# Optimization experiments

Measured on AMD Instinct MI355X. Metric: run time of the kernel, lower is better.

Reference implementation:

```python
import jax, jax.numpy as jnp
import numpy as np

K_MASK = -2.3819763e+38
B, T, D = 1, 2048, 3584
N, KH, H = 28, 4, 128  # query heads, kv heads, head_dim
ROPE_THETA = 1000000.0


def _rope_tables(t, h, theta):
    pos = jnp.arange(t, dtype=jnp.float32)[:, None]
    freq = theta ** (-jnp.arange(0, h, 2, dtype=jnp.float32) / h)[None, :]
    ang = pos * freq  # (T, H/2)
    return jnp.sin(ang)[None], jnp.cos(ang)[None]  # (1, T, H/2)


def apply_rotary_embedding(x, sin, cos):
    # x: (B,T,heads,H); sin/cos: (B,T,H/2)
    x1, x2 = x[..., : x.shape[-1] // 2], x[..., x.shape[-1] // 2 :]
    s, c = sin[:, :, None, :], cos[:, :, None, :]
    return jnp.concatenate([x1 * c - x2 * s, x2 * c + x1 * s], axis=-1)


def setup_inputs() -> dict:
    key = jax.random.key(0)
    ks = jax.random.split(key, 8)
    x = jax.random.normal(ks[0], (B, T, D), jnp.float32)
    attn_mask = jnp.tril(jnp.ones((T, T), jnp.bool_))[None]  # causal (B,T,S)
    sin, cos = _rope_tables(T, H, ROPE_THETA)
    std = 0.02
    wq = jax.random.normal(ks[1], (D, N, H), jnp.float32) * std
    wk = jax.random.normal(ks[2], (D, KH, H), jnp.float32) * std
    wv = jax.random.normal(ks[3], (D, KH, H), jnp.float32) * std
    wo = jax.random.normal(ks[4], (N, H, D), jnp.float32) * std
    q_bias = jax.random.normal(ks[5], (N * H,), jnp.float32) * std
    k_bias = jax.random.normal(ks[6], (KH * H,), jnp.float32) * std
    v_bias = jax.random.normal(ks[7], (KH * H,), jnp.float32) * std
    return {"x": x, "attn_mask": attn_mask, "sin": sin, "cos": cos,
            "wq": wq, "wk": wk, "wv": wv, "wo": wo,
            "q_bias": q_bias, "k_bias": k_bias, "v_bias": v_bias}


def reference(x, attn_mask, sin, cos, wq, wk, wv, wo, q_bias, k_bias, v_bias):
    b, t, _ = x.shape
    q = jnp.einsum('BTD,DNH->BTNH', x, wq) + q_bias.reshape(1, 1, N, H)
    k = jnp.einsum('BSD,DKH->BSKH', x, wk) + k_bias.reshape(1, 1, KH, H)
    v = jnp.einsum('BSD,DKH->BSKH', x, wv) + v_bias.reshape(1, 1, KH, H)
    q = apply_rotary_embedding(q, sin, cos)
    k = apply_rotary_embedding(k, sin, cos)
    g = N // KH  # GQA group size
    scale = H ** -0.5
    qg = q.reshape(b, t, KH, g, H)
    attn = jnp.einsum('BTHGD,BSHD->BHGTS', qg, k) * scale  # no KV repetition
    attn = attn.reshape(b, N, t, t)
    attn = jnp.where(attn_mask[:, None, :, :], attn, K_MASK)
    attn = jax.nn.softmax(attn.astype(jnp.float32), axis=-1).astype(k.dtype)
    attn = attn.reshape(b, KH, g, t, t)
    qkv = jnp.einsum('BHGTS,BSHD->BTHGD', attn, v).reshape(b, t, N, H)
    return jnp.einsum('BTNH,NHD->BTD', qkv, wo)
```

## Files before the change

kernel.cpp:

```cpp
#include <hip/hip_runtime.h>
#include <hip/hip_bf16.h>
#include <math.h>

#define Tn 2048
#define Dn 3584
#define NH 28
#define KHn 4
#define Hn 128
#define Gn 7
#define SCALE 0.08838834764831845f
#define LDC 4608
#define KOFF 3584
#define VOFF 4096
#define FBQ 128
#define FBS 64
#define NSPLIT 2

typedef unsigned short u16;
typedef __attribute__((ext_vector_type(8))) short short8;
typedef __attribute__((ext_vector_type(4))) float floatx4;

__device__ __forceinline__ float bf_lo(unsigned int u) {
    union { unsigned int i; float f; } x; x.i = u << 16; return x.f;
}
__device__ __forceinline__ u16 f2bf(float f) {
    __hip_bfloat16 h = __float2bfloat16(f);
    return *reinterpret_cast<u16*>(&h);
}

__global__ void cast_f32_bf16(const float* __restrict__ in, u16* __restrict__ out, int n4)
{
    const int idx = blockIdx.x * blockDim.x + threadIdx.x;
    if (idx >= n4) return;
    const float4 f = ((const float4*)in)[idx];
    ((ushort4*)out)[idx] = make_ushort4(f2bf(f.x), f2bf(f.y), f2bf(f.z), f2bf(f.w));
}

__global__ __launch_bounds__(256) void transpose_cast(
    const float* __restrict__ in, u16* __restrict__ out, int R, int C, int ldo)
{
    __shared__ float ts[32][33];
    const int tid = threadIdx.x;
    const int c0 = blockIdx.x * 32, r0 = blockIdx.y * 32;
    const int tx = tid & 31, ty = tid >> 5;
    #pragma unroll
    for (int i = 0; i < 4; ++i)
        ts[ty + i * 8][tx] = in[(size_t)(r0 + ty + i * 8) * C + c0 + tx];
    __syncthreads();
    #pragma unroll
    for (int i = 0; i < 4; ++i)
        out[(size_t)(c0 + ty + i * 8) * ldo + r0 + tx] = f2bf(ts[tx][ty + i * 8]);
}

__global__ __launch_bounds__(256) void transpose_v(
    const u16* __restrict__ qkv, u16* __restrict__ vt)
{
    __shared__ u16 ts[32][33];
    const int tid = threadIdx.x;
    const int s0 = blockIdx.x * 32, d0 = blockIdx.y * 32;
    const int tx = tid & 31, ty = tid >> 5;
    #pragma unroll
    for (int i = 0; i < 4; ++i)
        ts[ty + i * 8][tx] = qkv[(size_t)(s0 + ty + i * 8) * LDC + VOFF + d0 + tx];
    __syncthreads();
    #pragma unroll
    for (int i = 0; i < 4; ++i)
        vt[(size_t)(d0 + ty + i * 8) * Tn + s0 + tx] = ts[tx][ty + i * 8];
}

__global__ void concat_bias(const float* __restrict__ qb, const float* __restrict__ kb,
                            const float* __restrict__ vb, float* __restrict__ out)
{
    const int j = blockIdx.x * blockDim.x + threadIdx.x;
    if (j >= 4608) return;
    out[j] = j < 3584 ? qb[j] : (j < 4096 ? kb[j - 3584] : vb[j - 4096]);
}

#define GM 128
#define GN 128
#define GK 32

__device__ __forceinline__ void async16(const void* g, void* l) {
    __builtin_amdgcn_global_load_lds(
        (const __attribute__((address_space(1))) unsigned int*)g,
        (__attribute__((address_space(3))) unsigned int*)l, 16, 0, 0);
}

template <typename OUT_T>
__global__ __launch_bounds__(256) void gemm_bf16_mfma(
    const u16* __restrict__ A, const u16* __restrict__ Bt,
    const float* __restrict__ bias, OUT_T* __restrict__ C,
    int M, int N, int K, int ldc)
{
    __shared__ __align__(16) u16 As[GM * GK];
    __shared__ __align__(16) u16 Bs[GN * GK];

    const int tid  = threadIdx.x;
    const int lane = tid & 63;
    const int wave = tid >> 6;
    const int wr = wave >> 1, wc = wave & 1;
    const int m16 = lane & 15, quad = lane >> 4;

    const int bm = blockIdx.y * GM;
    const int bn = blockIdx.x * GN;

    floatx4 acc[4][4];
    #pragma unroll
    for (int i = 0; i < 4; ++i)
        #pragma unroll
        for (int j = 0; j < 4; ++j) acc[i][j] = (floatx4)0.f;

    const int rl   = lane >> 2;
    const int kcol = (lane & 3) * 8;

    for (int k0 = 0; k0 < K; k0 += GK) {
        __syncthreads();
        #pragma unroll
        for (int i = 0; i < 2; ++i) {
            const int c = wave + i * 4;
            const int row = c * 16 + rl;
            async16(A  + (size_t)(bm + row) * K + k0 + kcol, &As[c * 512]);
            async16(Bt + (size_t)(bn + row) * K + k0 + kcol, &Bs[c * 512]);
        }
        __builtin_amdgcn_s_waitcnt(0);
        __syncthreads();

        short8 af[4], bfr[4];
        #pragma unroll
        for (int i = 0; i < 4; ++i)
            af[i] = *(const short8*)&As[(wr * 64 + i * 16 + m16) * GK + quad * 8];
        #pragma unroll
        for (int j = 0; j < 4; ++j)
            bfr[j] = *(const short8*)&Bs[(wc * 64 + j * 16 + m16) * GK + quad * 8];
        #pragma unroll
        for (int i = 0; i < 4; ++i)
            #pragma unroll
            for (int j = 0; j < 4; ++j)
                acc[i][j] = __builtin_amdgcn_mfma_f32_16x16x32_bf16(
                    af[i], bfr[j], acc[i][j], 0, 0, 0);
    }

    #pragma unroll
    for (int j = 0; j < 4; ++j) {
        const int col = bn + wc * 64 + j * 16 + m16;
        const float bv = bias ? bias[col] : 0.f;
        #pragma unroll
        for (int i = 0; i < 4; ++i) {
            const int rbase = bm + wr * 64 + i * 16 + quad * 4;
            #pragma unroll
            for (int r = 0; r < 4; ++r) {
                const float v = acc[i][j][r] + bv;
                if constexpr (sizeof(OUT_T) == 2)
                    C[(size_t)(rbase + r) * ldc + col] = (OUT_T)f2bf(v);
                else
                    C[(size_t)(rbase + r) * ldc + col] = v;
            }
        }
    }
}

__global__ void rope_bf16(u16* __restrict__ base,
                          const float* __restrict__ sin_t,
                          const float* __restrict__ cos_t,
                          int heads)
{
    const int idx = blockIdx.x * blockDim.x + threadIdx.x;
    const int n_elem = Tn * heads * 64;
    if (idx >= n_elem) return;
    const int i = idx & 63;
    const int h = (idx >> 6) % heads;
    const int t = idx / (64 * heads);
    const float s = sin_t[t * 64 + i];
    const float c = cos_t[t * 64 + i];
    u16* p = base + (size_t)t * LDC + h * Hn;
    const float x1 = bf_lo((unsigned int)p[i]);
    const float x2 = bf_lo((unsigned int)p[i + 64]);
    p[i]      = f2bf(x1 * c - x2 * s);
    p[i + 64] = f2bf(x2 * c + x1 * s);
}

__global__ __launch_bounds__(256, 2) void flash_attn_mfma(
    const u16* __restrict__ qkv, const u16* __restrict__ vt,
    float* __restrict__ po0, float* __restrict__ po1,
    float2* __restrict__ ml)
{
    const int qt = (int)(gridDim.x - 1 - blockIdx.x);
    const int n  = blockIdx.y;
    const int z  = blockIdx.z;
    const int kh = n / Gn;
    const int tid  = threadIdx.x;
    const int lane = tid & 63;
    const int w    = tid >> 6;
    const int m16  = lane & 15;
    const int quad = lane >> 4;

    __shared__ __align__(16) u16 smem[64 * 136 + 128 * 72 + 128 * 72];
    u16* Ks = smem;
    u16* Vs = smem + 64 * 136;
    u16* Ps = Vs + 128 * 72;

    short8 qf[2][4];
    #pragma unroll
    for (int p = 0; p < 2; ++p) {
        const int qrow = qt * FBQ + w * 32 + p * 16 + m16;
        const u16* qp = qkv + (size_t)qrow * LDC + n * Hn;
        #pragma unroll
        for (int kc = 0; kc < 4; ++kc)
            qf[p][kc] = *(const short8*)(qp + kc * 32 + quad * 8);
    }

    floatx4 oacc[2][8];
    #pragma unroll
    for (int p = 0; p < 2; ++p)
        #pragma unroll
        for (int jn = 0; jn < 8; ++jn) oacc[p][jn] = (floatx4)0.f;
    float mrow[2][4], lrow[2][4];
    #pragma unroll
    for (int p = 0; p < 2; ++p)
        #pragma unroll
        for (int r = 0; r < 4; ++r) { mrow[p][r] = -3.0e38f; lrow[p][r] = 0.f; }

    const int krow = tid >> 2, kseg = tid & 3;
    const int vrow = tid >> 1, vseg = tid & 1;
    const int st0 = z * (qt + 1);
    const int st1 = st0 + qt + 1;

    uint4 kv[4], vv[4];
    {
        const u16* kp = qkv + (size_t)(st0 * FBS + krow) * LDC + KOFF + kh * Hn + kseg * 32;
        #pragma unroll
        for (int i = 0; i < 4; ++i) kv[i] = *(const uint4*)(kp + i * 8);
        const u16* vp = vt + (size_t)(kh * Hn + vrow) * Tn + st0 * FBS + vseg * 32;
        #pragma unroll
        for (int i = 0; i < 4; ++i) vv[i] = *(const uint4*)(vp + i * 8);
    }

    for (int st = st0; st < st1; ++st) {
        __syncthreads();
        #pragma unroll
        for (int i = 0; i < 4; ++i)
            *(uint4*)&Ks[krow * 136 + kseg * 32 + i * 8] = kv[i];
        #pragma unroll
        for (int i = 0; i < 4; ++i)
            *(uint4*)&Vs[vrow * 72 + vseg * 32 + i * 8] = vv[i];
        __syncthreads();

        {
            const int pst = (st + 1 < st1) ? st + 1 : st1 - 1;
            const u16* kp = qkv + (size_t)(pst * FBS + krow) * LDC + KOFF + kh * Hn + kseg * 32;
            #pragma unroll
            for (int i = 0; i < 4; ++i) kv[i] = *(const uint4*)(kp + i * 8);
            const u16* vp = vt + (size_t)(kh * Hn + vrow) * Tn + pst * FBS + vseg * 32;
            #pragma unroll
            for (int i = 0; i < 4; ++i) vv[i] = *(const uint4*)(vp + i * 8);
        }

        const bool active = (st * FBS) <= (qt * FBQ + w * 32 + 31);
        if (active) {
            floatx4 sacc[2][4];
            #pragma unroll
            for (int p = 0; p < 2; ++p)
                #pragma unroll
                for (int j = 0; j < 4; ++j) sacc[p][j] = (floatx4)0.f;
            #pragma unroll
            for (int j = 0; j < 4; ++j) {
                #pragma unroll
                for (int kc = 0; kc < 4; ++kc) {
                    const short8 bfv = *(const short8*)&Ks[(j * 16 + m16) * 136 + kc * 32 + quad * 8];
                    sacc[0][j] = __builtin_amdgcn_mfma_f32_16x16x32_bf16(qf[0][kc], bfv, sacc[0][j], 0, 0, 0);
                    sacc[1][j] = __builtin_amdgcn_mfma_f32_16x16x32_bf16(qf[1][kc], bfv, sacc[1][j], 0, 0, 0);
                }
            }

            const bool diag = (st >= 2 * qt);
            #pragma unroll
            for (int p = 0; p < 2; ++p) {
                #pragma unroll
                for (int r = 0; r < 4; ++r) {
                    const int prow = w * 32 + p * 16 + quad * 4 + r;
                    const int row  = qt * FBQ + prow;
                    float sv[4];
                    #pragma unroll
                    for (int j = 0; j < 4; ++j) {
                        float s = sacc[p][j][r] * SCALE;
                        if (diag && (st * FBS + j * 16 + m16 > row)) s = -1.0e30f;
                        sv[j] = s;
                    }
                    float mx = fmaxf(fmaxf(sv[0], sv[1]), fmaxf(sv[2], sv[3]));
                    mx = fmaxf(mx, __shfl_xor(mx, 1));
                    mx = fmaxf(mx, __shfl_xor(mx, 2));
                    mx = fmaxf(mx, __shfl_xor(mx, 4));
                    mx = fmaxf(mx, __shfl_xor(mx, 8));
                    const float mnew  = fmaxf(mrow[p][r], mx);
                    const float alpha = __expf(mrow[p][r] - mnew);
                    mrow[p][r] = mnew;
                    float ls = 0.f;
                    #pragma unroll
                    for (int j = 0; j < 4; ++j) {
                        const float e = __expf(sv[j] - mnew);
                        ls += e;
                        Ps[prow * 72 + j * 16 + m16] = f2bf(e);
                    }
                    lrow[p][r] = lrow[p][r] * alpha + ls;
                    #pragma unroll
                    for (int jn = 0; jn < 8; ++jn) oacc[p][jn][r] *= alpha;
                }
            }

            #pragma unroll
            for (int kc2 = 0; kc2 < 2; ++kc2) {
                const short8 af0 = *(const short8*)&Ps[(w * 32 + m16) * 72 + kc2 * 32 + quad * 8];
                const short8 af1 = *(const short8*)&Ps[(w * 32 + 16 + m16) * 72 + kc2 * 32 + quad * 8];
                #pragma unroll
                for (int jn = 0; jn < 8; ++jn) {
                    const short8 bfv = *(const short8*)&Vs[(jn * 16 + m16) * 72 + kc2 * 32 + quad * 8];
                    oacc[0][jn] = __builtin_amdgcn_mfma_f32_16x16x32_bf16(af0, bfv, oacc[0][jn], 0, 0, 0);
                    oacc[1][jn] = __builtin_amdgcn_mfma_f32_16x16x32_bf16(af1, bfv, oacc[1][jn], 0, 0, 0);
                }
            }
        }
    }

    float lsum[2][4];
    #pragma unroll
    for (int p = 0; p < 2; ++p)
        #pragma unroll
        for (int r = 0; r < 4; ++r) {
            float l = lrow[p][r];
            l += __shfl_xor(l, 1); l += __shfl_xor(l, 2);
            l += __shfl_xor(l, 4); l += __shfl_xor(l, 8);
            lsum[p][r] = l;
        }

    if (m16 == 0) {
        #pragma unroll
        for (int p = 0; p < 2; ++p)
            #pragma unroll
            for (int r = 0; r < 4; ++r) {
                const int row = qt * FBQ + w * 32 + p * 16 + quad * 4 + r;
                ml[((size_t)z * NH + n) * Tn + row] = make_float2(mrow[p][r], lsum[p][r]);
            }
    }

    float* po = z ? po1 : po0;
    #pragma unroll
    for (int p = 0; p < 2; ++p)
        #pragma unroll
        for (int r = 0; r < 4; ++r) {
            const int grow = qt * FBQ + w * 32 + p * 16 + quad * 4 + r;
            float* pr = po + (size_t)grow * Dn + n * Hn + m16;
            #pragma unroll
            for (int jn = 0; jn < 8; ++jn)
                pr[jn * 16] = oacc[p][jn][r];
        }
}

__global__ __launch_bounds__(256) void combine_splits(
    const float* __restrict__ po0, const float* __restrict__ po1,
    const float2* __restrict__ ml, u16* __restrict__ ob)
{
    const int idx = blockIdx.x * blockDim.x + threadIdx.x;
    const int n4  = Tn * Dn / 4;
    if (idx >= n4) return;
    const int c4  = idx % (Dn / 4);
    const int row = idx / (Dn / 4);
    const int n   = (c4 * 4) / Hn;

    const float2 ml0 = ml[(size_t)n * Tn + row];
    const float2 ml1 = ml[(size_t)(NH + n) * Tn + row];
    const float  M   = fmaxf(ml0.x, ml1.x);
    const float  a0  = __expf(ml0.x - M);
    const float  a1  = __expf(ml1.x - M);
    const float  dn_ = 1.0f / (ml0.y * a0 + ml1.y * a1);

    const float4 v0 = ((const float4*)po0)[idx];
    const float4 v1 = ((const float4*)po1)[idx];
    ushort4 o;
    o.x = f2bf((v0.x * a0 + v1.x * a1) * dn_);
    o.y = f2bf((v0.y * a0 + v1.y * a1) * dn_);
    o.z = f2bf((v0.z * a0 + v1.z * a1) * dn_);
    o.w = f2bf((v0.w * a0 + v1.w * a1) * dn_);
    ((ushort4*)ob)[idx] = o;
}

extern "C" void kernel_launch(void* const* d_in, const int* in_sizes, int n_in,
                              void* d_out, int out_size, void* d_ws, size_t ws_size,
                              hipStream_t stream)
{
    const float* x      = (const float*)d_in[0];
    const float* sin_t  = (const float*)d_in[2];
    const float* cos_t  = (const float*)d_in[3];
    const float* wq     = (const float*)d_in[4];
    const float* wk     = (const float*)d_in[5];
    const float* wv     = (const float*)d_in[6];
    const float* wo     = (const float*)d_in[7];
    const float* q_bias = (const float*)d_in[8];
    const float* k_bias = (const float*)d_in[9];
    const float* v_bias = (const float*)d_in[10];
    float* out = (float*)d_out;

    char* ws = (char*)d_ws;
    u16*  cqkv = (u16*)ws;
    u16*  abuf = (u16*)(ws + 18874368);
    u16*  wt   = (u16*)(ws + 18874368 + 14680064);
    float* bqkv = (float*)(ws + 66584576);
    u16*  vtg  = wt;
    float* po0 = (float*)d_out;
    float* po1 = (float*)(ws + 35651584);
    float2* mlb = (float2*)(ws + 65011712);
    u16*  xb   = (u16*)d_out;

    cast_f32_bf16<<<(Tn * Dn / 4 + 255) / 256, 256, 0, stream>>>(x, xb, Tn * Dn / 4);
    transpose_cast<<<dim3(Dn / 32, Dn / 32), 256, 0, stream>>>(wq, wt, Dn, Dn, Dn);
    transpose_cast<<<dim3(512 / 32, Dn / 32), 256, 0, stream>>>(wk, wt + (size_t)KOFF * Dn, Dn, 512, Dn);
    transpose_cast<<<dim3(512 / 32, Dn / 32), 256, 0, stream>>>(wv, wt + (size_t)VOFF * Dn, Dn, 512, Dn);
    concat_bias<<<18, 256, 0, stream>>>(q_bias, k_bias, v_bias, bqkv);

    gemm_bf16_mfma<u16><<<dim3(LDC / GN, Tn / GM), 256, 0, stream>>>(
        xb, wt, bqkv, cqkv, Tn, LDC, Dn, LDC);

    rope_bf16<<<(Tn * 32 * 64 + 255) / 256, 256, 0, stream>>>(cqkv, sin_t, cos_t, 32);

    transpose_v<<<dim3(Tn / 32, 512 / 32), 256, 0, stream>>>(cqkv, vtg);

    flash_attn_mfma<<<dim3(Tn / FBQ, NH, NSPLIT), 256, 0, stream>>>(
        cqkv, vtg, po0, po1, mlb);

    combine_splits<<<(Tn * Dn / 4 + 255) / 256, 256, 0, stream>>>(po0, po1, mlb, abuf);

    transpose_cast<<<dim3(Dn / 32, Dn / 32), 256, 0, stream>>>(wo, wt, Dn, Dn, Dn);
    gemm_bf16_mfma<float><<<dim3(Dn / GN, Tn / GM), 256, 0, stream>>>(
        abuf, wt, nullptr, out, Tn, Dn, Dn, Dn);
}
```

Measured before the change: 621.0 us.

## Load K/V MFMA fragments directly from global memory, drop LDS staging

The flash attention kernel no longer stages K and V tiles through shared memory with register prefetch and two barriers per tile. Each wave now reads its MFMA B-operand fragments straight from global memory (relying on L1/L2 caching), keeping only the P tile in LDS. This removes the block-wide syncs and cuts LDS use, which could raise occupancy and let waves skip inactive tiles independently. The cost is that every wave refetches the same K/V data, the loads are strided and uncoalesced, and the software prefetch that hid their latency is gone.

```diff
diff --git a/kernel.cpp b/kernel.cpp
--- a/kernel.cpp
+++ b/kernel.cpp
@@ -194,10 +194,7 @@
     const int m16  = lane & 15;
     const int quad = lane >> 4;
 
-    __shared__ __align__(16) u16 smem[64 * 136 + 128 * 72 + 128 * 72];
-    u16* Ks = smem;
-    u16* Vs = smem + 64 * 136;
-    u16* Ps = Vs + 128 * 72;
+    __shared__ __align__(16) u16 Ps[128 * 72];
 
     short8 qf[2][4];
     #pragma unroll
@@ -220,103 +217,77 @@
         #pragma unroll
         for (int r = 0; r < 4; ++r) { mrow[p][r] = -3.0e38f; lrow[p][r] = 0.f; }
 
-    const int krow = tid >> 2, kseg = tid & 3;
-    const int vrow = tid >> 1, vseg = tid & 1;
     const int st0 = z * (qt + 1);
     const int st1 = st0 + qt + 1;
 
-    uint4 kv[4], vv[4];
-    {
-        const u16* kp = qkv + (size_t)(st0 * FBS + krow) * LDC + KOFF + kh * Hn + kseg * 32;
-        #pragma unroll
-        for (int i = 0; i < 4; ++i) kv[i] = *(const uint4*)(kp + i * 8);
-        const u16* vp = vt + (size_t)(kh * Hn + vrow) * Tn + st0 * FBS + vseg * 32;
-        #pragma unroll
-        for (int i = 0; i < 4; ++i) vv[i] = *(const uint4*)(vp + i * 8);
-    }
+    const u16* kfrag = qkv + (size_t)m16 * LDC + KOFF + kh * Hn + quad * 8;
+    const u16* vfrag = vt + (size_t)(kh * Hn + m16) * Tn + quad * 8;
 
     for (int st = st0; st < st1; ++st) {
-        __syncthreads();
-        #pragma unroll
-        for (int i = 0; i < 4; ++i)
-            *(uint4*)&Ks[krow * 136 + kseg * 32 + i * 8] = kv[i];
-        #pragma unroll
-        for (int i = 0; i < 4; ++i)
-            *(uint4*)&Vs[vrow * 72 + vseg * 32 + i * 8] = vv[i];
-        __syncthreads();
-
-        {
-            const int pst = (st + 1 < st1) ? st + 1 : st1 - 1;
-            const u16* kp = qkv + (size_t)(pst * FBS + krow) * LDC + KOFF + kh * Hn + kseg * 32;
-            #pragma unroll
-            for (int i = 0; i < 4; ++i) kv[i] = *(const uint4*)(kp + i * 8);
-            const u16* vp = vt + (size_t)(kh * Hn + vrow) * Tn + pst * FBS + vseg * 32;
-            #pragma unroll
-            for (int i = 0; i < 4; ++i) vv[i] = *(const uint4*)(vp + i * 8);
-        }
-
-        const bool active = (st * FBS) <= (qt * FBQ + w * 32 + 31);
-        if (active) {
-            floatx4 sacc[2][4];
-            #pragma unroll
-            for (int p = 0; p < 2; ++p)
+        if ((st * FBS) > (qt * FBQ + w * 32 + 31)) continue;
+
+        const u16* kb = kfrag + (size_t)(st * FBS) * LDC;
+        const u16* vb = vfrag + st * FBS;
+
+        floatx4 sacc[2][4];
+        #pragma unroll
+        for (int j = 0; j < 4; ++j) sacc[0][j] = (floatx4)0.f;
+        #pragma unroll
+        for (int j = 0; j < 4; ++j) sacc[1][j] = (floatx4)0.f;
+        #pragma unroll
+        for (int j = 0; j < 4; ++j) {
+            #pragma unroll
+            for (int kc = 0; kc < 4; ++kc) {
+                const short8 bfv = *(const short8*)(kb + (size_t)(j * 16) * LDC + kc * 32);
+                sacc[0][j] = __builtin_amdgcn_mfma_f32_16x16x32_bf16(qf[0][kc], bfv, sacc[0][j], 0, 0, 0);
+                sacc[1][j] = __builtin_amdgcn_mfma_f32_16x16x32_bf16(qf[1][kc], bfv, sacc[1][j], 0, 0, 0);
+            }
+        }
+
+        const bool diag = (st >= 2 * qt);
+        #pragma unroll
+        for (int p = 0; p < 2; ++p) {
+            #pragma unroll
+            for (int r = 0; r < 4; ++r) {
+                const int prow = w * 32 + p * 16 + quad * 4 + r;
+                const int row  = qt * FBQ + prow;
+                float sv[4];
                 #pragma unroll
-                for (int j = 0; j < 4; ++j) sacc[p][j] = (floatx4)0.f;
-            #pragma unroll
-            for (int j = 0; j < 4; ++j) {
+                for (int j = 0; j < 4; ++j) {
+                    float s = sacc[p][j][r] * SCALE;
+                    if (diag && (st * FBS + j * 16 + m16 > row)) s = -1.0e30f;
+                    sv[j] = s;
+                }
+                float mx = fmaxf(fmaxf(sv[0], sv[1]), fmaxf(sv[2], sv[3]));
+                mx = fmaxf(mx, __shfl_xor(mx, 1));
+                mx = fmaxf(mx, __shfl_xor(mx, 2));
+                mx = fmaxf(mx, __shfl_xor(mx, 4));
+                mx = fmaxf(mx, __shfl_xor(mx, 8));
+                const float mnew  = fmaxf(mrow[p][r], mx);
+                const float alpha = __expf(mrow[p][r] - mnew);
+                mrow[p][r] = mnew;
+                float ls = 0.f;
                 #pragma unroll
-                for (int kc = 0; kc < 4; ++kc) {
-                    const short8 bfv = *(const short8*)&Ks[(j * 16 + m16) * 136 + kc * 32 + quad * 8];
-                    sacc[0][j] = __builtin_amdgcn_mfma_f32_16x16x32_bf16(qf[0][kc], bfv, sacc[0][j], 0, 0, 0);
-                    sacc[1][j] = __builtin_amdgcn_mfma_f32_16x16x32_bf16(qf[1][kc], bfv, sacc[1][j], 0, 0, 0);
+                for (int j = 0; j < 4; ++j) {
+                    const float e = __expf(sv[j] - mnew);
+                    ls += e;
+                    Ps[prow * 72 + j * 16 + m16] = f2bf(e);
                 }
+                lrow[p][r] = lrow[p][r] * alpha + ls;
+                #pragma unroll
+                for (int jn = 0; jn < 8; ++jn) oacc[p][jn][r] *= alpha;
             }
-
-            const bool diag = (st >= 2 * qt);
-            #pragma unroll
-            for (int p = 0; p < 2; ++p) {
-                #pragma unroll
-                for (int r = 0; r < 4; ++r) {
-                    const int prow = w * 32 + p * 16 + quad * 4 + r;
-                    const int row  = qt * FBQ + prow;
-                    float sv[4];
-                    #pragma unroll
-                    for (int j = 0; j < 4; ++j) {
-                        float s = sacc[p][j][r] * SCALE;
-                        if (diag && (st * FBS + j * 16 + m16 > row)) s = -1.0e30f;
-                        sv[j] = s;
-                    }
-                    float mx = fmaxf(fmaxf(sv[0], sv[1]), fmaxf(sv[2], sv[3]));
-                    mx = fmaxf(mx, __shfl_xor(mx, 1));
-                    mx = fmaxf(mx, __shfl_xor(mx, 2));
-                    mx = fmaxf(mx, __shfl_xor(mx, 4));
-                    mx = fmaxf(mx, __shfl_xor(mx, 8));
-                    const float mnew  = fmaxf(mrow[p][r], mx);
-                    const float alpha = __expf(mrow[p][r] - mnew);
-                    mrow[p][r] = mnew;
-                    float ls = 0.f;
-                    #pragma unroll
-                    for (int j = 0; j < 4; ++j) {
-                        const float e = __expf(sv[j] - mnew);
-                        ls += e;
-                        Ps[prow * 72 + j * 16 + m16] = f2bf(e);
-                    }
-                    lrow[p][r] = lrow[p][r] * alpha + ls;
-                    #pragma unroll
-                    for (int jn = 0; jn < 8; ++jn) oacc[p][jn][r] *= alpha;
-                }
-            }
-
-            #pragma unroll
-            for (int kc2 = 0; kc2 < 2; ++kc2) {
-                const short8 af0 = *(const short8*)&Ps[(w * 32 + m16) * 72 + kc2 * 32 + quad * 8];
-                const short8 af1 = *(const short8*)&Ps[(w * 32 + 16 + m16) * 72 + kc2 * 32 + quad * 8];
-                #pragma unroll
-                for (int jn = 0; jn < 8; ++jn) {
-                    const short8 bfv = *(const short8*)&Vs[(jn * 16 + m16) * 72 + kc2 * 32 + quad * 8];
-                    oacc[0][jn] = __builtin_amdgcn_mfma_f32_16x16x32_bf16(af0, bfv, oacc[0][jn], 0, 0, 0);
-                    oacc[1][jn] = __builtin_amdgcn_mfma_f32_16x16x32_bf16(af1, bfv, oacc[1][jn], 0, 0, 0);
-                }
+        }
+
+        #pragma unroll
+        for (int kc2 = 0; kc2 < 2; ++kc2) {
+            const short8 af0 = *(const short8*)&Ps[(w * 32 + m16) * 72 + kc2 * 32 + quad * 8];
+            const short8 af1 = *(const short8*)&Ps[(w * 32 + 16 + m16) * 72 + kc2 * 32 + quad * 8];
+            #pragma unroll
+            for (int jn = 0; jn < 8; ++jn) {
+                const short8 bfv = *(const short8*)(vb + (size_t)(jn * 16) * Tn + kc2 * 32);
+                oacc[0][jn] = __builtin_amdgcn_mfma_f32_16x16x32_bf16(af0, bfv, oacc[0][jn], 0, 0, 0);
+                oacc[1][jn] = __builtin_amdgcn_mfma_f32_16x16x32_bf16(af1, bfv, oacc[1][jn], 0, 0, 0);
             }
         }
     }
```

After: 656.8 us. 1.06x slower.
